# Kernel tuning notes

Hardware: AMD Instinct MI355X
Metric: run time of the kernel (lower is better)

## Reference

```python
import jax, jax.numpy as jnp
import numpy as np


def setup_inputs() -> dict:
    key = jax.random.key(0)
    k1, k2 = jax.random.split(key)
    bsz, n_views, d = 4096, 2, 512
    features = jax.random.normal(k1, (bsz, n_views, d), dtype=jnp.float32)
    labels = jax.random.randint(k2, (bsz,), 0, 100)
    return {"features": features, "labels": labels}


def reference(features, labels):
    # Faithful vectorization of Fourdloss.forward (contrast_mode='all').
    bsz, n_views, d = features.shape
    N = bsz * n_views
    # torch.cat(torch.unbind(features, dim=1), dim=0): view-major stacking
    cf = jnp.transpose(features, (1, 0, 2)).reshape(N, d)  # contrast == anchor feature
    lab = jnp.tile(labels, n_views)                        # labels2[i] = labels[i % bsz]
    same = lab[:, None] == lab[None, :]                    # [N, N]
    neg = ~same                                            # mask2
    negf = neg.astype(jnp.float32)
    # positive mask with diagonal removed (mask * logits_mask)
    pos_mask = same.astype(jnp.float32) * (1.0 - jnp.eye(N, dtype=jnp.float32))

    # pairwise dot products with the hardcoded 0.035 temperature
    D = (cf @ cf.T) / 0.035                                # [N, N], D[m, j] = c_m . a_j / 0.035

    # Inner loop over j: over rows m with labels2[m] != labels2[j],
    # S[j] = sum_m exp(D[m, j] - max_m D[m, j])
    maxd = jnp.max(jnp.where(neg, D, -jnp.inf), axis=0)    # [N], per-column masked max
    z = jnp.where(neg, D - maxd[None, :], 0.0)             # safe: masked entries -> exp(0)*0
    S = jnp.sum(jnp.exp(z) * negf, axis=0)                 # [N]

    # Outer loop over i: sum S[j] over all j that are negatives of i; k = count
    num = negf @ S                                         # negtive_dot_negtive_sum
    negcount = negf.sum(axis=1)                            # negtivesum (k)
    x = num / negcount                                     # [N] (repeated across columns in torch)
    log_prob = -jnp.log(x + 1e-12)                         # constant per row

    pos_count = pos_mask.sum(axis=1)
    mask_sum = jnp.where(pos_count == 0, 1.0, pos_count)
    # (mask * log_prob).sum(1) == log_prob * pos_count since log_prob is row-constant
    pos_logits = -(pos_count * log_prob) / mask_sum
    loss = pos_logits.reshape(n_views, bsz).mean()
    return loss
```

## Files before the change

kernel.cpp:

```cpp
#include <hip/hip_runtime.h>

typedef unsigned short u16;
typedef unsigned int u32;
typedef __attribute__((ext_vector_type(8))) short bfrag;
typedef __attribute__((ext_vector_type(4))) float facc;

#define N 8192
#define DIM 512
#define BM 128
#define BK 32
#define NK (DIM / BK)
#define NTILE 2080
#define NPART 64
#define NCLS 100
#define TPX 260

#if __has_builtin(__builtin_amdgcn_exp2f)
#define EXP2(x) __builtin_amdgcn_exp2f(x)
#else
#define EXP2(x) exp2f(x)
#endif

__device__ __forceinline__ u16 f2bf(float f) {
  u32 u = __float_as_uint(f);
  u32 r = u + 0x7fffu + ((u >> 16) & 1u);
  return (u16)(r >> 16);
}
__device__ __forceinline__ float bf2f(u16 h) {
  return __uint_as_float(((u32)h) << 16);
}

__global__ void prep_kernel(const float* __restrict__ F, u16* __restrict__ Ahi,
                            u16* __restrict__ Alo, float* __restrict__ classSum,
                            int* __restrict__ classCnt)
{
  const float sc = sqrtf(1.4426950408889634f / 0.035f);
  int idx = (blockIdx.x * 256 + threadIdx.x) * 4;
  float4 x = *(const float4*)(F + idx);
  float v[4] = {x.x * sc, x.y * sc, x.z * sc, x.w * sc};
  u16 h[4], l[4];
#pragma unroll
  for (int i = 0; i < 4; ++i) {
    h[i] = f2bf(v[i]);
    l[i] = f2bf(v[i] - bf2f(h[i]));
  }
  *(ushort4*)(Ahi + idx) = make_ushort4(h[0], h[1], h[2], h[3]);
  *(ushort4*)(Alo + idx) = make_ushort4(l[0], l[1], l[2], l[3]);
  if (blockIdx.x == 0 && threadIdx.x < NCLS) {
    classSum[threadIdx.x] = 0.f;
    classCnt[threadIdx.x] = 0;
  }
}

__device__ __forceinline__ void stage16(const u16* g, u16* l) {
  __builtin_amdgcn_global_load_lds((const __attribute__((address_space(1))) void*)g,
                                   (__attribute__((address_space(3))) void*)l, 16, 0, 0);
}

__device__ __forceinline__ void mergeMS(float& m, float& s, float m2, float s2) {
  float M = fmaxf(m, m2);
  s = s * EXP2(m - M) + s2 * EXP2(m2 - M);
  m = M;
}

__global__ __launch_bounds__(256, 2) void gram_flash(
    const u16* __restrict__ Ahi, const u16* __restrict__ Alo,
    const int* __restrict__ labels,
    float* __restrict__ m_part, float* __restrict__ s_part)
{
  __shared__ __align__(16) u16 lds[2][4 * BM * BK];
  __shared__ float mbuf[1024];

  const int tid = threadIdx.x;
  const int wave = tid >> 6;
  const int lane = tid & 63;
  const int wr = wave >> 1, wc = wave & 1;
  const int l15 = lane & 15, lg = lane >> 4;

  const int t = (blockIdx.x & 7) * TPX + (blockIdx.x >> 3);
  int SI = 0, base = 0;
  for (;; ++SI) {
    int rowcnt = 36 + (7 - SI) * 64;
    if (t < base + rowcnt) break;
    base += rowcnt;
  }
  const int r = t - base;
  int SJ, li, lj;
  if (r < 36) {
    SJ = SI;
    int a = 0, cum = 0;
    for (;; ++a) { if (r < cum + (8 - a)) break; cum += 8 - a; }
    li = a; lj = a + (r - cum);
  } else {
    int rr = r - 36;
    SJ = SI + 1 + (rr >> 6);
    li = (rr & 63) >> 3;
    lj = rr & 7;
  }
  const int I = SI * 8 + li, J = SJ * 8 + lj;
  const int i0 = I * BM;
  const int j0 = J * BM;

  u32 lr[4];
#pragma unroll
  for (int mi = 0; mi < 4; ++mi) {
    u32 pk = 0;
#pragma unroll
    for (int rg = 0; rg < 4; ++rg) {
      int rr2 = i0 + wr * 64 + mi * 16 + lg * 4 + rg;
      pk |= ((u32)labels[rr2 >> 1] & 0xffu) << (8 * rg);
    }
    lr[mi] = pk;
  }
  int lc[4];
#pragma unroll
  for (int ni = 0; ni < 4; ++ni)
    lc[ni] = labels[(j0 + wc * 64 + ni * 16 + l15) >> 1];

  facc acc[4][4];
#pragma unroll
  for (int a = 0; a < 4; ++a)
#pragma unroll
    for (int b = 0; b < 4; ++b)
      acc[a][b] = (facc){0.f, 0.f, 0.f, 0.f};

  auto STAGE = [&](int kk, int b) {
    u16* d_ahi = &lds[b][0];
    u16* d_alo = &lds[b][BM * BK];
    u16* d_bhi = &lds[b][2 * BM * BK];
    u16* d_blo = &lds[b][3 * BM * BK];
    const int k0 = kk * BK;
#pragma unroll
    for (int q = 0; q < 2; ++q) {
      const int ci = (wave * 2 + q) * 64 + lane;
      const int L = ci >> 3;
      const int sc2 = ci & 7;
      const int cb = sc2 ^ (L & 7);
      const int row = L * 2 + (cb >> 2);
      const int kc = cb & 3;
      const size_t goffA = (size_t)(i0 + row) * DIM + k0 + kc * 8;
      const size_t goffB = (size_t)(j0 + row) * DIM + k0 + kc * 8;
      const int lbase = (wave * 2 + q) * 512;
      stage16(Ahi + goffA, d_ahi + lbase);
      stage16(Alo + goffA, d_alo + lbase);
      stage16(Ahi + goffB, d_bhi + lbase);
      stage16(Alo + goffB, d_blo + lbase);
    }
  };

  STAGE(0, 0);
  STAGE(1, 1);

  for (int k = 0; k < NK; ++k) {
    const int cur = k & 1;
    if (k + 1 < NK)
      asm volatile("s_waitcnt vmcnt(8)" ::: "memory");
    else
      asm volatile("s_waitcnt vmcnt(0)" ::: "memory");
    __builtin_amdgcn_s_barrier();

    const u16* lb_ahi = &lds[cur][0];
    const u16* lb_alo = &lds[cur][BM * BK];
    const u16* lb_bhi = &lds[cur][2 * BM * BK];
    const u16* lb_blo = &lds[cur][3 * BM * BK];

    bfrag fah[4], fal[4], fbh[4], fbl[4];
#pragma unroll
    for (int mi = 0; mi < 4; ++mi) {
      const int row = wr * 64 + mi * 16 + l15;
      const int L = row >> 1;
      const int cb = ((row & 1) << 2) | lg;
      const int off = L * 64 + (cb ^ (L & 7)) * 8;
      fah[mi] = *(const bfrag*)(lb_ahi + off);
      fal[mi] = *(const bfrag*)(lb_alo + off);
    }
#pragma unroll
    for (int ni = 0; ni < 4; ++ni) {
      const int row = wc * 64 + ni * 16 + l15;
      const int L = row >> 1;
      const int cb = ((row & 1) << 2) | lg;
      const int off = L * 64 + (cb ^ (L & 7)) * 8;
      fbh[ni] = *(const bfrag*)(lb_bhi + off);
      fbl[ni] = *(const bfrag*)(lb_blo + off);
    }
#pragma unroll
    for (int mi = 0; mi < 4; ++mi)
#pragma unroll
      for (int ni = 0; ni < 4; ++ni)
        acc[mi][ni] = __builtin_amdgcn_mfma_f32_16x16x32_bf16(fah[mi], fbh[ni], acc[mi][ni], 0, 0, 0);
#pragma unroll
    for (int mi = 0; mi < 4; ++mi)
#pragma unroll
      for (int ni = 0; ni < 4; ++ni)
        acc[mi][ni] = __builtin_amdgcn_mfma_f32_16x16x32_bf16(fah[mi], fbl[ni], acc[mi][ni], 0, 0, 0);
#pragma unroll
    for (int mi = 0; mi < 4; ++mi)
#pragma unroll
      for (int ni = 0; ni < 4; ++ni)
        acc[mi][ni] = __builtin_amdgcn_mfma_f32_16x16x32_bf16(fal[mi], fbh[ni], acc[mi][ni], 0, 0, 0);

    if (k + 2 < NK) {
      __builtin_amdgcn_s_barrier();
      STAGE(k + 2, cur);
    }
  }

#pragma unroll
  for (int mi = 0; mi < 4; ++mi)
#pragma unroll
    for (int rg = 0; rg < 4; ++rg) {
      const int labr = (int)((lr[mi] >> (8 * rg)) & 0xffu);
#pragma unroll
      for (int ni = 0; ni < 4; ++ni)
        if (labr == lc[ni]) acc[mi][ni][rg] = -1e30f;
    }

  float rm[16], rs[16];
#pragma unroll
  for (int mi = 0; mi < 4; ++mi)
#pragma unroll
    for (int rg = 0; rg < 4; ++rg) {
      const int si = mi * 4 + rg;
      float m = -1e20f;
#pragma unroll
      for (int ni = 0; ni < 4; ++ni) m = fmaxf(m, acc[mi][ni][rg]);
      float s = 0.f;
#pragma unroll
      for (int ni = 0; ni < 4; ++ni) s += EXP2(acc[mi][ni][rg] - m);
      rm[si] = m; rs[si] = s;
    }
#pragma unroll
  for (int st = 1; st <= 8; st <<= 1)
#pragma unroll
    for (int si = 0; si < 16; ++si)
      mergeMS(rm[si], rs[si], __shfl_xor(rm[si], st, 64), __shfl_xor(rs[si], st, 64));

  float cm[4], cs[4];
#pragma unroll
  for (int ni = 0; ni < 4; ++ni) {
    float m = -1e20f;
#pragma unroll
    for (int mi = 0; mi < 4; ++mi)
#pragma unroll
      for (int rg = 0; rg < 4; ++rg) m = fmaxf(m, acc[mi][ni][rg]);
    float s = 0.f;
#pragma unroll
    for (int mi = 0; mi < 4; ++mi)
#pragma unroll
      for (int rg = 0; rg < 4; ++rg) s += EXP2(acc[mi][ni][rg] - m);
    cm[ni] = m; cs[ni] = s;
  }
#pragma unroll
  for (int st = 16; st <= 32; st <<= 1)
#pragma unroll
    for (int ni = 0; ni < 4; ++ni)
      mergeMS(cm[ni], cs[ni], __shfl_xor(cm[ni], st, 64), __shfl_xor(cs[ni], st, 64));

  float* RM = mbuf;
  float* RS = mbuf + 256;
  float* CM = mbuf + 512;
  float* CS = mbuf + 768;

  __syncthreads();
  if (l15 == 0) {
#pragma unroll
    for (int mi = 0; mi < 4; ++mi)
#pragma unroll
      for (int rg = 0; rg < 4; ++rg) {
        const int idx = wr * 64 + mi * 16 + lg * 4 + rg;
        RM[wc * 128 + idx] = rm[mi * 4 + rg];
        RS[wc * 128 + idx] = rs[mi * 4 + rg];
      }
  }
  if (lg == 0 && I != J) {
#pragma unroll
    for (int ni = 0; ni < 4; ++ni) {
      const int c = wc * 64 + ni * 16 + l15;
      CM[wr * 128 + c] = cm[ni];
      CS[wr * 128 + c] = cs[ni];
    }
  }
  __syncthreads();

  if (tid < 128) {
    float m = RM[tid], s = RS[tid];
    mergeMS(m, s, RM[128 + tid], RS[128 + tid]);
    m_part[(size_t)J * N + i0 + tid] = m;
    s_part[(size_t)J * N + i0 + tid] = s;
  } else if (I != J) {
    const int c = tid - 128;
    float m = CM[c], s = CS[c];
    mergeMS(m, s, CM[128 + c], CS[128 + c]);
    m_part[(size_t)I * N + j0 + c] = m;
    s_part[(size_t)I * N + j0 + c] = s;
  }
}

__global__ void combine_kernel(const float* __restrict__ m_part,
                               const float* __restrict__ s_part,
                               const int* __restrict__ labels,
                               float* __restrict__ classSum,
                               int* __restrict__ classCnt)
{
  __shared__ float MB[4][64], SB[4][64];
  const int jloc = threadIdx.x & 63;
  const int pc = threadIdx.x >> 6;
  const int j = blockIdx.x * 64 + jloc;
  float M = -1e20f, S = 0.f;
  for (int p = pc * 16; p < pc * 16 + 16; ++p)
    mergeMS(M, S, m_part[(size_t)p * N + j], s_part[(size_t)p * N + j]);
  MB[pc][jloc] = M; SB[pc][jloc] = S;
  __syncthreads();
  if (pc == 0) {
#pragma unroll
    for (int q = 1; q < 4; ++q) mergeMS(M, S, MB[q][jloc], SB[q][jloc]);
    int c = labels[j >> 1];
    atomicAdd(&classSum[c], S);
    atomicAdd(&classCnt[c], 1);
  }
}

__global__ void final_kernel(const float* __restrict__ classSum,
                             const int* __restrict__ classCnt,
                             float* __restrict__ out)
{
  __shared__ float red[128];
  int t = threadIdx.x;
  float total = 0.f;
  for (int c = 0; c < NCLS; ++c) total += classSum[c];
  float term = 0.f;
  if (t < NCLS) {
    int cnt = classCnt[t];
    if (cnt > 0) {
      float x = (total - classSum[t]) / (float)(N - cnt) + 1e-12f;
      term = (float)cnt * logf(x);
    }
  }
  red[t] = term;
  __syncthreads();
  for (int s = 64; s > 0; s >>= 1) {
    if (t < s) red[t] += red[t + s];
    __syncthreads();
  }
  if (t == 0) out[0] = red[0] / (float)N;
}

extern "C" void kernel_launch(void* const* d_in, const int* in_sizes, int n_in,
                              void* d_out, int out_size, void* d_ws, size_t ws_size,
                              hipStream_t stream)
{
  (void)in_sizes; (void)n_in; (void)out_size; (void)ws_size;
  const float* F = (const float*)d_in[0];
  const int* labels = (const int*)d_in[1];
  float* out = (float*)d_out;

  char* ws = (char*)d_ws;
  u16* Ahi = (u16*)ws;
  u16* Alo = (u16*)(ws + (size_t)N * DIM * 2);
  float* m_part = (float*)(ws + (size_t)N * DIM * 4);
  float* s_part = m_part + (size_t)NPART * N;
  float* classSum = s_part + (size_t)NPART * N;
  int* classCnt = (int*)(classSum + NCLS);

  prep_kernel<<<(N * DIM) / 1024, 256, 0, stream>>>(F, Ahi, Alo, classSum, classCnt);
  gram_flash<<<NTILE, 256, 0, stream>>>(Ahi, Alo, labels, m_part, s_part);
  combine_kernel<<<N / 64, 256, 0, stream>>>(m_part, s_part, labels, classSum, classCnt);
  final_kernel<<<1, 128, 0, stream>>>(classSum, classCnt, out);
}
```

Baseline: 217.4 us.

## Make gram kernel persistent with contiguous tile ranges and running row stats

```diff
diff --git a/kernel.cpp b/kernel.cpp
--- a/kernel.cpp
+++ b/kernel.cpp
@@ -13,7 +13,7 @@
 #define NTILE 2080
 #define NPART 64
 #define NCLS 100
-#define TPX 260
+#define NBLK 512
 
 #if __has_builtin(__builtin_amdgcn_exp2f)
 #define EXP2(x) __builtin_amdgcn_exp2f(x)
@@ -31,8 +31,9 @@
 }
 
 __global__ void prep_kernel(const float* __restrict__ F, u16* __restrict__ Ahi,
-                            u16* __restrict__ Alo, float* __restrict__ classSum,
-                            int* __restrict__ classCnt)
+                            u16* __restrict__ Alo, float* __restrict__ m_part,
+                            float* __restrict__ s_part,
+                            float* __restrict__ classSum, int* __restrict__ classCnt)
 {
   const float sc = sqrtf(1.4426950408889634f / 0.035f);
   int idx = (blockIdx.x * 256 + threadIdx.x) * 4;
@@ -46,6 +47,11 @@
   }
   *(ushort4*)(Ahi + idx) = make_ushort4(h[0], h[1], h[2], h[3]);
   *(ushort4*)(Alo + idx) = make_ushort4(l[0], l[1], l[2], l[3]);
+  int pidx = blockIdx.x * 256 + threadIdx.x;
+  if (pidx < NPART * N) {
+    m_part[pidx] = -1e30f;
+    s_part[pidx] = 0.f;
+  }
   if (blockIdx.x == 0 && threadIdx.x < NCLS) {
     classSum[threadIdx.x] = 0.f;
     classCnt[threadIdx.x] = 0;
@@ -77,222 +83,261 @@
   const int wr = wave >> 1, wc = wave & 1;
   const int l15 = lane & 15, lg = lane >> 4;
 
-  const int t = (blockIdx.x & 7) * TPX + (blockIdx.x >> 3);
-  int SI = 0, base = 0;
-  for (;; ++SI) {
-    int rowcnt = 36 + (7 - SI) * 64;
-    if (t < base + rowcnt) break;
-    base += rowcnt;
-  }
-  const int r = t - base;
-  int SJ, li, lj;
-  if (r < 36) {
-    SJ = SI;
-    int a = 0, cum = 0;
-    for (;; ++a) { if (r < cum + (8 - a)) break; cum += 8 - a; }
-    li = a; lj = a + (r - cum);
-  } else {
-    int rr = r - 36;
-    SJ = SI + 1 + (rr >> 6);
-    li = (rr & 63) >> 3;
-    lj = rr & 7;
-  }
-  const int I = SI * 8 + li, J = SJ * 8 + lj;
-  const int i0 = I * BM;
-  const int j0 = J * BM;
-
+  const int sidx = (blockIdx.x & 7) * 64 + (blockIdx.x >> 3);
+  const int tstart = (sidx * NTILE) >> 9;
+  const int tend = ((sidx + 1) * NTILE) >> 9;
+
+  float rm[16], rs[16];
+  int curI = -1, i0c = 0, Jseg = 0;
   u32 lr[4];
-#pragma unroll
-  for (int mi = 0; mi < 4; ++mi) {
-    u32 pk = 0;
-#pragma unroll
-    for (int rg = 0; rg < 4; ++rg) {
-      int rr2 = i0 + wr * 64 + mi * 16 + lg * 4 + rg;
-      pk |= ((u32)labels[rr2 >> 1] & 0xffu) << (8 * rg);
-    }
-    lr[mi] = pk;
-  }
-  int lc[4];
-#pragma unroll
-  for (int ni = 0; ni < 4; ++ni)
-    lc[ni] = labels[(j0 + wc * 64 + ni * 16 + l15) >> 1];
-
-  facc acc[4][4];
-#pragma unroll
-  for (int a = 0; a < 4; ++a)
-#pragma unroll
-    for (int b = 0; b < 4; ++b)
-      acc[a][b] = (facc){0.f, 0.f, 0.f, 0.f};
-
-  auto STAGE = [&](int kk, int b) {
-    u16* d_ahi = &lds[b][0];
-    u16* d_alo = &lds[b][BM * BK];
-    u16* d_bhi = &lds[b][2 * BM * BK];
-    u16* d_blo = &lds[b][3 * BM * BK];
-    const int k0 = kk * BK;
-#pragma unroll
-    for (int q = 0; q < 2; ++q) {
-      const int ci = (wave * 2 + q) * 64 + lane;
-      const int L = ci >> 3;
-      const int sc2 = ci & 7;
-      const int cb = sc2 ^ (L & 7);
-      const int row = L * 2 + (cb >> 2);
-      const int kc = cb & 3;
-      const size_t goffA = (size_t)(i0 + row) * DIM + k0 + kc * 8;
-      const size_t goffB = (size_t)(j0 + row) * DIM + k0 + kc * 8;
-      const int lbase = (wave * 2 + q) * 512;
-      stage16(Ahi + goffA, d_ahi + lbase);
-      stage16(Alo + goffA, d_alo + lbase);
-      stage16(Ahi + goffB, d_bhi + lbase);
-      stage16(Alo + goffB, d_blo + lbase);
-    }
-  };
-
-  STAGE(0, 0);
-  STAGE(1, 1);
-
-  for (int k = 0; k < NK; ++k) {
-    const int cur = k & 1;
-    if (k + 1 < NK)
-      asm volatile("s_waitcnt vmcnt(8)" ::: "memory");
-    else
-      asm volatile("s_waitcnt vmcnt(0)" ::: "memory");
-    __builtin_amdgcn_s_barrier();
-
-    const u16* lb_ahi = &lds[cur][0];
-    const u16* lb_alo = &lds[cur][BM * BK];
-    const u16* lb_bhi = &lds[cur][2 * BM * BK];
-    const u16* lb_blo = &lds[cur][3 * BM * BK];
-
-    bfrag fah[4], fal[4], fbh[4], fbl[4];
-#pragma unroll
-    for (int mi = 0; mi < 4; ++mi) {
-      const int row = wr * 64 + mi * 16 + l15;
-      const int L = row >> 1;
-      const int cb = ((row & 1) << 2) | lg;
-      const int off = L * 64 + (cb ^ (L & 7)) * 8;
-      fah[mi] = *(const bfrag*)(lb_ahi + off);
-      fal[mi] = *(const bfrag*)(lb_alo + off);
-    }
-#pragma unroll
-    for (int ni = 0; ni < 4; ++ni) {
-      const int row = wc * 64 + ni * 16 + l15;
-      const int L = row >> 1;
-      const int cb = ((row & 1) << 2) | lg;
-      const int off = L * 64 + (cb ^ (L & 7)) * 8;
-      fbh[ni] = *(const bfrag*)(lb_bhi + off);
-      fbl[ni] = *(const bfrag*)(lb_blo + off);
-    }
-#pragma unroll
-    for (int mi = 0; mi < 4; ++mi)
-#pragma unroll
-      for (int ni = 0; ni < 4; ++ni)
-        acc[mi][ni] = __builtin_amdgcn_mfma_f32_16x16x32_bf16(fah[mi], fbh[ni], acc[mi][ni], 0, 0, 0);
-#pragma unroll
-    for (int mi = 0; mi < 4; ++mi)
-#pragma unroll
-      for (int ni = 0; ni < 4; ++ni)
-        acc[mi][ni] = __builtin_amdgcn_mfma_f32_16x16x32_bf16(fah[mi], fbl[ni], acc[mi][ni], 0, 0, 0);
-#pragma unroll
-    for (int mi = 0; mi < 4; ++mi)
-#pragma unroll
-      for (int ni = 0; ni < 4; ++ni)
-        acc[mi][ni] = __builtin_amdgcn_mfma_f32_16x16x32_bf16(fal[mi], fbh[ni], acc[mi][ni], 0, 0, 0);
-
-    if (k + 2 < NK) {
-      __builtin_amdgcn_s_barrier();
-      STAGE(k + 2, cur);
-    }
-  }
-
-#pragma unroll
-  for (int mi = 0; mi < 4; ++mi)
-#pragma unroll
-    for (int rg = 0; rg < 4; ++rg) {
-      const int labr = (int)((lr[mi] >> (8 * rg)) & 0xffu);
-#pragma unroll
-      for (int ni = 0; ni < 4; ++ni)
-        if (labr == lc[ni]) acc[mi][ni][rg] = -1e30f;
-    }
-
-  float rm[16], rs[16];
-#pragma unroll
-  for (int mi = 0; mi < 4; ++mi)
-#pragma unroll
-    for (int rg = 0; rg < 4; ++rg) {
-      const int si = mi * 4 + rg;
-      float m = -1e20f;
-#pragma unroll
-      for (int ni = 0; ni < 4; ++ni) m = fmaxf(m, acc[mi][ni][rg]);
-      float s = 0.f;
-#pragma unroll
-      for (int ni = 0; ni < 4; ++ni) s += EXP2(acc[mi][ni][rg] - m);
-      rm[si] = m; rs[si] = s;
-    }
-#pragma unroll
-  for (int st = 1; st <= 8; st <<= 1)
-#pragma unroll
-    for (int si = 0; si < 16; ++si)
-      mergeMS(rm[si], rs[si], __shfl_xor(rm[si], st, 64), __shfl_xor(rs[si], st, 64));
-
-  float cm[4], cs[4];
-#pragma unroll
-  for (int ni = 0; ni < 4; ++ni) {
-    float m = -1e20f;
-#pragma unroll
-    for (int mi = 0; mi < 4; ++mi)
-#pragma unroll
-      for (int rg = 0; rg < 4; ++rg) m = fmaxf(m, acc[mi][ni][rg]);
-    float s = 0.f;
-#pragma unroll
-    for (int mi = 0; mi < 4; ++mi)
-#pragma unroll
-      for (int rg = 0; rg < 4; ++rg) s += EXP2(acc[mi][ni][rg] - m);
-    cm[ni] = m; cs[ni] = s;
-  }
-#pragma unroll
-  for (int st = 16; st <= 32; st <<= 1)
-#pragma unroll
-    for (int ni = 0; ni < 4; ++ni)
-      mergeMS(cm[ni], cs[ni], __shfl_xor(cm[ni], st, 64), __shfl_xor(cs[ni], st, 64));
 
   float* RM = mbuf;
   float* RS = mbuf + 256;
   float* CM = mbuf + 512;
   float* CS = mbuf + 768;
 
-  __syncthreads();
-  if (l15 == 0) {
+  for (int t = tstart; t < tend; ++t) {
+    int SI = 0, base = 0;
+    for (;; ++SI) {
+      int rowcnt = 36 + (7 - SI) * 64;
+      if (t < base + rowcnt) break;
+      base += rowcnt;
+    }
+    const int r = t - base;
+    int SJ, li, lj;
+    if (r < 36) {
+      SJ = SI;
+      int a = 0, cum = 0;
+      for (;; ++a) { if (r < cum + (8 - a)) break; cum += 8 - a; }
+      li = a; lj = a + (r - cum);
+    } else {
+      int rr = r - 36;
+      SJ = SI + 1 + (rr >> 6);
+      li = (rr & 63) >> 3;
+      lj = rr & 7;
+    }
+    const int I = SI * 8 + li, J = SJ * 8 + lj;
+    const int i0 = I * BM;
+    const int j0 = J * BM;
+
+    if (I != curI) {
+      if (curI >= 0) {
+#pragma unroll
+        for (int st = 1; st <= 8; st <<= 1)
+#pragma unroll
+          for (int si = 0; si < 16; ++si)
+            mergeMS(rm[si], rs[si], __shfl_xor(rm[si], st, 64), __shfl_xor(rs[si], st, 64));
+        __syncthreads();
+        if (l15 == 0) {
+#pragma unroll
+          for (int mi = 0; mi < 4; ++mi)
+#pragma unroll
+            for (int rg = 0; rg < 4; ++rg) {
+              const int idx = wr * 64 + mi * 16 + lg * 4 + rg;
+              RM[wc * 128 + idx] = rm[mi * 4 + rg];
+              RS[wc * 128 + idx] = rs[mi * 4 + rg];
+            }
+        }
+        __syncthreads();
+        if (tid < 128) {
+          float m = RM[tid], s = RS[tid];
+          mergeMS(m, s, RM[128 + tid], RS[128 + tid]);
+          m_part[(size_t)Jseg * N + i0c + tid] = m;
+          s_part[(size_t)Jseg * N + i0c + tid] = s;
+        }
+      }
+      curI = I; i0c = i0; Jseg = J;
+#pragma unroll
+      for (int si = 0; si < 16; ++si) { rm[si] = -1e30f; rs[si] = 0.f; }
+#pragma unroll
+      for (int mi = 0; mi < 4; ++mi) {
+        u32 pk = 0;
+#pragma unroll
+        for (int rg = 0; rg < 4; ++rg) {
+          int rr2 = i0 + wr * 64 + mi * 16 + lg * 4 + rg;
+          pk |= ((u32)labels[rr2 >> 1] & 0xffu) << (8 * rg);
+        }
+        lr[mi] = pk;
+      }
+    }
+
+    int lc[4];
+#pragma unroll
+    for (int ni = 0; ni < 4; ++ni)
+      lc[ni] = labels[(j0 + wc * 64 + ni * 16 + l15) >> 1];
+
+    facc acc[4][4];
+#pragma unroll
+    for (int a = 0; a < 4; ++a)
+#pragma unroll
+      for (int b = 0; b < 4; ++b)
+        acc[a][b] = (facc){0.f, 0.f, 0.f, 0.f};
+
+    auto STAGE = [&](int kk, int b) {
+      u16* d_ahi = &lds[b][0];
+      u16* d_alo = &lds[b][BM * BK];
+      u16* d_bhi = &lds[b][2 * BM * BK];
+      u16* d_blo = &lds[b][3 * BM * BK];
+      const int k0 = kk * BK;
+#pragma unroll
+      for (int q = 0; q < 2; ++q) {
+        const int ci = (wave * 2 + q) * 64 + lane;
+        const int L = ci >> 3;
+        const int sc2 = ci & 7;
+        const int cb = sc2 ^ (L & 7);
+        const int row = L * 2 + (cb >> 2);
+        const int kc = cb & 3;
+        const size_t goffA = (size_t)(i0 + row) * DIM + k0 + kc * 8;
+        const size_t goffB = (size_t)(j0 + row) * DIM + k0 + kc * 8;
+        const int lbase = (wave * 2 + q) * 512;
+        stage16(Ahi + goffA, d_ahi + lbase);
+        stage16(Alo + goffA, d_alo + lbase);
+        stage16(Ahi + goffB, d_bhi + lbase);
+        stage16(Alo + goffB, d_blo + lbase);
+      }
+    };
+
+    STAGE(0, 0);
+    STAGE(1, 1);
+
+    for (int k = 0; k < NK; ++k) {
+      const int cur = k & 1;
+      if (k + 1 < NK)
+        asm volatile("s_waitcnt vmcnt(8)" ::: "memory");
+      else
+        asm volatile("s_waitcnt vmcnt(0)" ::: "memory");
+      __builtin_amdgcn_s_barrier();
+
+      const u16* lb_ahi = &lds[cur][0];
+      const u16* lb_alo = &lds[cur][BM * BK];
+      const u16* lb_bhi = &lds[cur][2 * BM * BK];
+      const u16* lb_blo = &lds[cur][3 * BM * BK];
+
+      bfrag fah[4], fal[4], fbh[4], fbl[4];
+#pragma unroll
+      for (int mi = 0; mi < 4; ++mi) {
+        const int row = wr * 64 + mi * 16 + l15;
+        const int L = row >> 1;
+        const int cb = ((row & 1) << 2) | lg;
+        const int off = L * 64 + (cb ^ (L & 7)) * 8;
+        fah[mi] = *(const bfrag*)(lb_ahi + off);
+        fal[mi] = *(const bfrag*)(lb_alo + off);
+      }
+#pragma unroll
+      for (int ni = 0; ni < 4; ++ni) {
+        const int row = wc * 64 + ni * 16 + l15;
+        const int L = row >> 1;
+        const int cb = ((row & 1) << 2) | lg;
+        const int off = L * 64 + (cb ^ (L & 7)) * 8;
+        fbh[ni] = *(const bfrag*)(lb_bhi + off);
+        fbl[ni] = *(const bfrag*)(lb_blo + off);
+      }
+#pragma unroll
+      for (int mi = 0; mi < 4; ++mi)
+#pragma unroll
+        for (int ni = 0; ni < 4; ++ni)
+          acc[mi][ni] = __builtin_amdgcn_mfma_f32_16x16x32_bf16(fah[mi], fbh[ni], acc[mi][ni], 0, 0, 0);
+#pragma unroll
+      for (int mi = 0; mi < 4; ++mi)
+#pragma unroll
+        for (int ni = 0; ni < 4; ++ni)
+          acc[mi][ni] = __builtin_amdgcn_mfma_f32_16x16x32_bf16(fah[mi], fbl[ni], acc[mi][ni], 0, 0, 0);
+#pragma unroll
+      for (int mi = 0; mi < 4; ++mi)
+#pragma unroll
+        for (int ni = 0; ni < 4; ++ni)
+          acc[mi][ni] = __builtin_amdgcn_mfma_f32_16x16x32_bf16(fal[mi], fbh[ni], acc[mi][ni], 0, 0, 0);
+
+      if (k + 2 < NK) {
+        __builtin_amdgcn_s_barrier();
+        STAGE(k + 2, cur);
+      }
+    }
+
 #pragma unroll
     for (int mi = 0; mi < 4; ++mi)
 #pragma unroll
       for (int rg = 0; rg < 4; ++rg) {
-        const int idx = wr * 64 + mi * 16 + lg * 4 + rg;
-        RM[wc * 128 + idx] = rm[mi * 4 + rg];
-        RS[wc * 128 + idx] = rs[mi * 4 + rg];
-      }
-  }
-  if (lg == 0 && I != J) {
-#pragma unroll
-    for (int ni = 0; ni < 4; ++ni) {
-      const int c = wc * 64 + ni * 16 + l15;
-      CM[wr * 128 + c] = cm[ni];
-      CS[wr * 128 + c] = cs[ni];
-    }
-  }
-  __syncthreads();
-
-  if (tid < 128) {
-    float m = RM[tid], s = RS[tid];
-    mergeMS(m, s, RM[128 + tid], RS[128 + tid]);
-    m_part[(size_t)J * N + i0 + tid] = m;
-    s_part[(size_t)J * N + i0 + tid] = s;
-  } else if (I != J) {
-    const int c = tid - 128;
-    float m = CM[c], s = CS[c];
-    mergeMS(m, s, CM[128 + c], CS[128 + c]);
-    m_part[(size_t)I * N + j0 + c] = m;
-    s_part[(size_t)I * N + j0 + c] = s;
+        const int si = mi * 4 + rg;
+        const int labr = (int)((lr[mi] >> (8 * rg)) & 0xffu);
+        float v0 = (labr == lc[0]) ? -1e30f : acc[mi][0][rg];
+        float v1 = (labr == lc[1]) ? -1e30f : acc[mi][1][rg];
+        float v2 = (labr == lc[2]) ? -1e30f : acc[mi][2][rg];
+        float v3 = (labr == lc[3]) ? -1e30f : acc[mi][3][rg];
+        acc[mi][0][rg] = v0; acc[mi][1][rg] = v1;
+        acc[mi][2][rg] = v2; acc[mi][3][rg] = v3;
+        float lm = fmaxf(fmaxf(v0, v1), fmaxf(v2, v3));
+        float M = fmaxf(rm[si], lm);
+        float fac = EXP2(rm[si] - M);
+        rs[si] = rs[si] * fac + ((EXP2(v0 - M) + EXP2(v1 - M)) + (EXP2(v2 - M) + EXP2(v3 - M)));
+        rm[si] = M;
+      }
+
+    __syncthreads();
+    if (I != J) {
+      float cm[4], cs[4];
+#pragma unroll
+      for (int ni = 0; ni < 4; ++ni) {
+        float m = -1e30f;
+#pragma unroll
+        for (int mi = 0; mi < 4; ++mi)
+#pragma unroll
+          for (int rg = 0; rg < 4; ++rg) m = fmaxf(m, acc[mi][ni][rg]);
+        float s = 0.f;
+#pragma unroll
+        for (int mi = 0; mi < 4; ++mi)
+#pragma unroll
+          for (int rg = 0; rg < 4; ++rg) s += EXP2(acc[mi][ni][rg] - m);
+        cm[ni] = m; cs[ni] = s;
+      }
+#pragma unroll
+      for (int st = 16; st <= 32; st <<= 1)
+#pragma unroll
+        for (int ni = 0; ni < 4; ++ni)
+          mergeMS(cm[ni], cs[ni], __shfl_xor(cm[ni], st, 64), __shfl_xor(cs[ni], st, 64));
+      if (lg == 0) {
+#pragma unroll
+        for (int ni = 0; ni < 4; ++ni) {
+          const int c = wc * 64 + ni * 16 + l15;
+          CM[wr * 128 + c] = cm[ni];
+          CS[wr * 128 + c] = cs[ni];
+        }
+      }
+    }
+    __syncthreads();
+    if (I != J && tid < 128) {
+      float m = CM[tid], s = CS[tid];
+      mergeMS(m, s, CM[128 + tid], CS[128 + tid]);
+      m_part[(size_t)I * N + j0 + tid] = m;
+      s_part[(size_t)I * N + j0 + tid] = s;
+    }
+    __syncthreads();
+  }
+
+  if (curI >= 0) {
+#pragma unroll
+    for (int st = 1; st <= 8; st <<= 1)
+#pragma unroll
+      for (int si = 0; si < 16; ++si)
+        mergeMS(rm[si], rs[si], __shfl_xor(rm[si], st, 64), __shfl_xor(rs[si], st, 64));
+    __syncthreads();
+    if (l15 == 0) {
+#pragma unroll
+      for (int mi = 0; mi < 4; ++mi)
+#pragma unroll
+        for (int rg = 0; rg < 4; ++rg) {
+          const int idx = wr * 64 + mi * 16 + lg * 4 + rg;
+          RM[wc * 128 + idx] = rm[mi * 4 + rg];
+          RS[wc * 128 + idx] = rs[mi * 4 + rg];
+        }
+    }
+    __syncthreads();
+    if (tid < 128) {
+      float m = RM[tid], s = RS[tid];
+      mergeMS(m, s, RM[128 + tid], RS[128 + tid]);
+      m_part[(size_t)Jseg * N + i0c + tid] = m;
+      s_part[(size_t)Jseg * N + i0c + tid] = s;
+    }
   }
 }
 
@@ -362,8 +407,9 @@
   float* classSum = s_part + (size_t)NPART * N;
   int* classCnt = (int*)(classSum + NCLS);
 
-  prep_kernel<<<(N * DIM) / 1024, 256, 0, stream>>>(F, Ahi, Alo, classSum, classCnt);
-  gram_flash<<<NTILE, 256, 0, stream>>>(Ahi, Alo, labels, m_part, s_part);
+  prep_kernel<<<(N * DIM) / 1024, 256, 0, stream>>>(F, Ahi, Alo, m_part, s_part,
+                                                    classSum, classCnt);
+  gram_flash<<<NBLK, 256, 0, stream>>>(Ahi, Alo, labels, m_part, s_part);
   combine_kernel<<<N / 64, 256, 0, stream>>>(m_part, s_part, labels, classSum, classCnt);
   final_kernel<<<1, 128, 0, stream>>>(classSum, classCnt, out);
 }
```

Result: slower. 235.4 us (+8.3%).
